# Kernel optimization log

Measured on AMD Instinct MI355X. Metric: run time of the kernel, lower is better.

## Reference

```python
import jax, jax.numpy as jnp
import numpy as np

N, C, H, W = 16, 64, 128, 128
SHIFT = 1  # frozen value of torch module's random.randint(-2, 2) drawn at __init__


def setup_inputs() -> dict:
    key = jax.random.key(0)
    k1, k2, k3 = jax.random.split(key, 3)
    x = jax.random.normal(k1, (N, C, H, W), dtype=jnp.float32)
    # p_3: Conv2d(c, c, (1,5), padding=(0,2), bias=False) -> weight (C_out, C_in, 1, 5)
    w3 = jax.random.normal(k2, (C, C, 1, 5), dtype=jnp.float32) * (1.0 / np.sqrt(5.0 * C))
    # p_7: Conv2d(9c, c, 1, groups=c, bias=False) -> per output channel, 9 input channels: (C, 9)
    w7 = jax.random.normal(k3, (C, 9), dtype=jnp.float32) * (1.0 / 3.0)
    return {"x": x, "w3": w3, "w7": w7}


def reference(x, w3, w7):
    n, c, h, w = x.shape
    # t_1: F.unfold(x, (1,3), dilation=(1,2), padding=(0,2)) -> width offsets -2, 0, +2 (zero padded)
    xp = jnp.pad(x, ((0, 0), (0, 0), (0, 0), (2, 2)))
    t1 = jnp.stack([xp[..., 0:w], xp[..., 2:w + 2], xp[..., 4:w + 4]], axis=2)  # (n,c,3,h,w)
    # t_3: 1x5 conv, padding (0,2)
    t3 = jax.lax.conv_general_dilated(
        x, w3, window_strides=(1, 1), padding=[(0, 0), (2, 2)],
        dimension_numbers=("NCHW", "OIHW", "NCHW"))  # (n,c,h,w)
    # t_4: F.unfold(t1 as (n,3c,h,w), (3,1), padding=(1,0)) -> height offsets -1, 0, +1
    t1p = jnp.pad(t1, ((0, 0), (0, 0), (0, 0), (1, 1), (0, 0)))
    t4 = jnp.stack([t1p[..., 0:h, :], t1p[..., 1:h + 1, :], t1p[..., 2:h + 2, :]],
                   axis=3)  # (n, c, 3[w_off], 3[h_off], h, w)
    # t_5: roll along the W axis (dim 5)
    t5 = jnp.roll(t4, SHIFT, axis=5)
    # t_6: maximum of lhs (n,c,1,3,h,w) and rhs (n,c,3,3,h,w); lhs offset dim aligns with rhs dim 3
    t6 = jnp.maximum(t1[:, :, None, :, :, :], t5)  # (n,c,3,3,h,w)
    # t_7: grouped 1x1 conv, groups=c, 9 input channels per group -> 1 output channel
    t6f = t6.reshape(n, c, 9, h, w)
    t7 = jnp.einsum("nckhw,ck->nchw", t6f, w7)
    return t7 * t3
```

## Files before the change

kernel.cpp:

```cpp
#include <hip/hip_runtime.h>

#define NN 16
#define CC 64
#define HH 128
#define WW 128

#define LDS_STRIDE 72
#define T3B_STRIDE 132

typedef __attribute__((ext_vector_type(8))) short short8;
typedef __attribute__((ext_vector_type(4))) float floatx4;

__device__ __forceinline__ short f2bf(float f) {
    union { float f; unsigned u; } v; v.f = f;
    unsigned r = v.u + 0x7fffu + ((v.u >> 16) & 1u);
    return (short)(r >> 16);
}
__device__ __forceinline__ unsigned pack2bf(float lo, float hi) {
    union { float f; unsigned u; } a, b; a.f = lo; b.f = hi;
    unsigned ra = a.u + 0x7fffu + ((a.u >> 16) & 1u);
    unsigned rb = b.u + 0x7fffu + ((b.u >> 16) & 1u);
    return (ra >> 16) | (rb & 0xffff0000u);
}
__device__ __forceinline__ float bf2f(unsigned short u) {
    union { unsigned u; float f; } v; v.u = ((unsigned)u) << 16;
    return v.f;
}

__global__ __launch_bounds__(256) void prep_w(const float* __restrict__ w3,
                                              short* __restrict__ Apk,
                                              float* __restrict__ zp) {
    int idx = blockIdx.x * 256 + threadIdx.x;
    if (idx < CC * 320) {
        int co = idx / 320;
        int kk = idx % 320;
        int mh = co >> 5, m = (co >> 4) & 1, lm = co & 15;
        int ks = kk >> 5, g = (kk >> 3) & 3, e = kk & 7;
        int tap = kk >> 6, ci = kk & 63;
        Apk[((((mh * 10 + ks) * 2 + m) * 64) + (g * 16 + lm)) * 8 + e] =
            f2bf(w3[(co * CC + ci) * 5 + tap]);
    }
    if (blockIdx.x == 0 && threadIdx.x < 64) zp[threadIdx.x] = 0.f;
}

__global__ __launch_bounds__(256, 6) void fused(const short* __restrict__ Apk,
                                                const float* __restrict__ x,
                                                const float* __restrict__ w7,
                                                const float* __restrict__ zp,
                                                float* __restrict__ out) {
    __shared__ __align__(16) char smem[19456];
    unsigned*    xsW  = (unsigned*)smem;
    const short* panel = (const short*)smem;
    short*       t3b  = (short*)smem;

    const int bid = blockIdx.x;
    const int nh  = ((bid & 7) << 8) | (bid >> 3);
    const int n   = nh >> 7;
    const int h   = nh & (HH - 1);
    const int tid = threadIdx.x;
    const int lane = tid & 63;
    const int W    = tid >> 6;

    {
        const int half = lane >> 5;
        const int wq   = lane & 31;
        const float* rowbase = x + ((size_t)n * CC * HH + h) * WW;
        #pragma unroll
        for (int i = 0; i < 4; ++i) {
            const int cp = W * 8 + i * 2 + half;
            const float* b0 = rowbase + (size_t)(2 * cp) * (HH * WW);
            float4 av = *(const float4*)(b0 + wq * 4);
            float4 bv = *(const float4*)(b0 + HH * WW + wq * 4);
            #pragma unroll
            for (int k = 0; k < 4; ++k) {
                int wp = wq * 4 + 2 + k;
                xsW[wp * 36 + cp] = pack2bf(av[k], bv[k]);
            }
        }
        if (tid < 128) {
            int wpi = tid >> 5;
            int wpz = (wpi < 2) ? wpi : 128 + wpi;
            xsW[wpz * 36 + (tid & 31)] = 0u;
        }
    }
    __syncthreads();

    const int lm = lane & 15;
    const int g  = lane >> 4;
    const int mh = W >> 1;
    const int wh = W & 1;

    floatx4 acc[2][4];
    #pragma unroll
    for (int m = 0; m < 2; ++m)
        #pragma unroll
        for (int j = 0; j < 4; ++j) acc[m][j] = (floatx4){0.f, 0.f, 0.f, 0.f};

    for (int ks = 0; ks < 10; ++ks) {
        const int kbase = ks * 32 + g * 8;
        const int tap   = kbase >> 6;
        const int cib   = kbase & 63;

        const short* ab = Apk + (((mh * 10 + ks) * 2) * 64 + lane) * 8;
        short8 a0 = *(const short8*)ab;
        short8 a1 = *(const short8*)(ab + 64 * 8);
        #pragma unroll
        for (int j = 0; j < 4; ++j) {
            int wp = (wh * 4 + j) * 16 + lm + tap;
            short8 b = *(const short8*)&panel[wp * LDS_STRIDE + cib];
            acc[0][j] = __builtin_amdgcn_mfma_f32_16x16x32_bf16(a0, b, acc[0][j], 0, 0, 0);
            acc[1][j] = __builtin_amdgcn_mfma_f32_16x16x32_bf16(a1, b, acc[1][j], 0, 0, 0);
        }
    }
    __syncthreads();

    #pragma unroll
    for (int m = 0; m < 2; ++m)
        #pragma unroll
        for (int j = 0; j < 4; ++j)
            #pragma unroll
            for (int r = 0; r < 4; ++r) {
                int co = (mh * 2 + m) * 16 + g * 4 + r;
                int w  = (wh * 4 + j) * 16 + lm;
                t3b[co * T3B_STRIDE + w] = f2bf(acc[m][j][r]);
            }

    const int w0   = (tid & 31) * 4;
    const int chi  = tid >> 5;
    const int lq31 = lane & 31;
    const bool isw = (lq31 == 0);
    const bool ise = (lq31 == 31);
    const int src31 = lane | 31;
    const int lsrc  = isw ? lane : lane - 1;
    const int rsrc  = ise ? lane : lane + 1;

    const float* pr[3]; int sr[3];
    const float* xb0 = x + (((size_t)(n * CC + chi)) * HH) * WW;
    #pragma unroll
    for (int r = 0; r < 3; ++r) {
        int hh = h + r - 1;
        bool hok = (unsigned)hh < HH;
        pr[r] = hok ? (xb0 + (size_t)hh * WW + w0) : zp;
        sr[r] = hok ? (8 * HH * WW) : 0;
    }
    const float* wcp = w7 + chi * 9;
    int t3o = chi * T3B_STRIDE + w0;
    float* outp = out + ((((size_t)(n * CC + chi)) * HH + h) * WW) + w0;

    __syncthreads();

    #define BUILD_WIN(dst, c)                                              \
        {                                                                  \
            float l1_ = __shfl((c).y, lsrc);                               \
            float l2_ = __shfl((c).z, lsrc);                               \
            float l3_ = __shfl((c).w, lsrc);                               \
            float r8_ = __shfl((c).x, rsrc);                               \
            float r9_ = __shfl((c).y, rsrc);                               \
            dst[1] = isw ? 0.f : l1_;                                      \
            dst[2] = isw ? 0.f : l2_;                                      \
            dst[3] = isw ? 0.f : l3_;                                      \
            dst[4] = (c).x; dst[5] = (c).y; dst[6] = (c).z; dst[7] = (c).w;\
            dst[8] = ise ? 0.f : r8_;                                      \
            dst[9] = ise ? 0.f : r9_;                                      \
        }

    #pragma unroll
    for (int it = 0; it < 8; ++it) {
        float4 cur[3];
        #pragma unroll
        for (int r = 0; r < 3; ++r) { cur[r] = *(const float4*)pr[r]; pr[r] += sr[r]; }
        float wc[9];
        #pragma unroll
        for (int t = 0; t < 9; ++t) wc[t] = wcp[t];
        ushort4 tv = *(const ushort4*)&t3b[t3o];

        float wrap0[3], wrap1[3];
        #pragma unroll
        for (int r = 0; r < 3; ++r) {
            wrap0[r] = __shfl(cur[r].y, src31);
            wrap1[r] = __shfl(cur[r].w, src31);
        }

        float win1[12];
        BUILD_WIN(win1, cur[1]);

        float t3v[4] = {bf2f(tv.x), bf2f(tv.y), bf2f(tv.z), bf2f(tv.w)};

        float res[4] = {0.f, 0.f, 0.f, 0.f};
        #pragma unroll
        for (int i = 0; i < 3; ++i) {
            float wini[12];
            if (i == 1) {
                #pragma unroll
                for (int t = 1; t < 10; ++t) wini[t] = win1[t];
            } else {
                BUILD_WIN(wini, cur[i]);
            }
            #pragma unroll
            for (int j = 0; j < 3; ++j) {
                #pragma unroll
                for (int e = 0; e < 4; ++e) {
                    float lhs = win1[e + 2 * i + 2];
                    float rhs = wini[e + 2 * j + 1];
                    if (e == 0)
                        rhs = isw ? ((j == 0) ? wrap0[i]
                                   : (j == 1) ? wrap1[i] : 0.f)
                                  : rhs;
                    res[e] = fmaf(wc[j * 3 + i], fmaxf(lhs, rhs), res[e]);
                }
            }
        }
        float4 o;
        o.x = res[0] * t3v[0]; o.y = res[1] * t3v[1];
        o.z = res[2] * t3v[2]; o.w = res[3] * t3v[3];
        *(float4*)outp = o;

        wcp  += 8 * 9;
        t3o  += 8 * T3B_STRIDE;
        outp += (size_t)8 * HH * WW;
    }
    #undef BUILD_WIN
}

extern "C" void kernel_launch(void* const* d_in, const int* in_sizes, int n_in,
                              void* d_out, int out_size, void* d_ws, size_t ws_size,
                              hipStream_t stream) {
    const float* x  = (const float*)d_in[0];
    const float* w3 = (const float*)d_in[1];
    const float* w7 = (const float*)d_in[2];
    float* out = (float*)d_out;

    short* Apk = (short*)d_ws;
    float* zp  = (float*)((char*)d_ws + 40960);

    prep_w<<<(CC * 320 + 255) / 256, 256, 0, stream>>>(w3, Apk, zp);
    fused<<<NN * HH, 256, 0, stream>>>(Apk, x, w7, zp, out);
}
```

Before: 140.3 us.

## Software-pipeline epilogue x loads, stage w7 in LDS, vectorize panel stores

The epilogue now issues the three x-row loads for the next channel group before computing the current one, using inline-asm global loads with explicit vmcnt waits. The first loads are issued before the barrier. The per-channel w7 weights are staged into LDS once per block and read back as vector loads instead of scalar global loads. The prologue loads 8 channels per thread and writes packed uint4 LDS stores instead of scalar ones. The manual waitcnt of 1 relies on the store-counter ordering, and the extra registers for double-buffering may lower occupancy.

Result: no change. 138.5 us (-1.3%).

```diff
diff --git a/kernel.cpp b/kernel.cpp
--- a/kernel.cpp
+++ b/kernel.cpp
@@ -7,6 +7,7 @@
 
 #define LDS_STRIDE 72
 #define T3B_STRIDE 132
+#define WCS_OFF    16896
 
 typedef __attribute__((ext_vector_type(8))) short short8;
 typedef __attribute__((ext_vector_type(4))) float floatx4;
@@ -25,6 +26,10 @@
 __device__ __forceinline__ float bf2f(unsigned short u) {
     union { unsigned u; float f; } v; v.u = ((unsigned)u) << 16;
     return v.f;
+}
+__device__ __forceinline__ void gload4(float4& d, const float* p) {
+    asm volatile("global_load_dwordx4 %0, %1, off"
+                 : "=&v"(d) : "v"(p) : "memory");
 }
 
 __global__ __launch_bounds__(256) void prep_w(const float* __restrict__ w3,
@@ -48,10 +53,11 @@
                                                 const float* __restrict__ w7,
                                                 const float* __restrict__ zp,
                                                 float* __restrict__ out) {
-    __shared__ __align__(16) char smem[19456];
+    __shared__ __align__(16) char smem[19968];
     unsigned*    xsW  = (unsigned*)smem;
     const short* panel = (const short*)smem;
     short*       t3b  = (short*)smem;
+    float*       wcs  = (float*)(smem + WCS_OFF);
 
     const int bid = blockIdx.x;
     const int nh  = ((bid & 7) << 8) | (bid >> 3);
@@ -64,18 +70,21 @@
     {
         const int half = lane >> 5;
         const int wq   = lane & 31;
-        const float* rowbase = x + ((size_t)n * CC * HH + h) * WW;
-        #pragma unroll
-        for (int i = 0; i < 4; ++i) {
-            const int cp = W * 8 + i * 2 + half;
-            const float* b0 = rowbase + (size_t)(2 * cp) * (HH * WW);
-            float4 av = *(const float4*)(b0 + wq * 4);
-            float4 bv = *(const float4*)(b0 + HH * WW + wq * 4);
-            #pragma unroll
-            for (int k = 0; k < 4; ++k) {
-                int wp = wq * 4 + 2 + k;
-                xsW[wp * 36 + cp] = pack2bf(av[k], bv[k]);
-            }
+        const int cp0  = W * 8 + half * 4;
+        const float* b0 = x + ((size_t)(n * CC + 2 * cp0) * HH + h) * WW;
+        float4 v[8];
+        #pragma unroll
+        for (int cc = 0; cc < 8; ++cc)
+            v[cc] = *(const float4*)(b0 + (size_t)cc * (HH * WW) + wq * 4);
+        #pragma unroll
+        for (int k = 0; k < 4; ++k) {
+            int wp = wq * 4 + 2 + k;
+            uint4 q;
+            q.x = pack2bf(v[0][k], v[1][k]);
+            q.y = pack2bf(v[2][k], v[3][k]);
+            q.z = pack2bf(v[4][k], v[5][k]);
+            q.w = pack2bf(v[6][k], v[7][k]);
+            *(uint4*)(xsW + wp * 36 + cp0) = q;
         }
         if (tid < 128) {
             int wpi = tid >> 5;
@@ -124,6 +133,15 @@
                 int w  = (wh * 4 + j) * 16 + lm;
                 t3b[co * T3B_STRIDE + w] = f2bf(acc[m][j][r]);
             }
+
+    if (tid < 144) {
+        float4 wv = *(const float4*)(w7 + tid * 4);
+        #pragma unroll
+        for (int e = 0; e < 4; ++e) {
+            int idx = tid * 4 + e;
+            wcs[(idx / 9) * 12 + (idx % 9)] = wv[e];
+        }
+    }
 
     const int w0   = (tid & 31) * 4;
     const int chi  = tid >> 5;
@@ -143,11 +161,17 @@
         pr[r] = hok ? (xb0 + (size_t)hh * WW + w0) : zp;
         sr[r] = hok ? (8 * HH * WW) : 0;
     }
-    const float* wcp = w7 + chi * 9;
     int t3o = chi * T3B_STRIDE + w0;
     float* outp = out + ((((size_t)(n * CC + chi)) * HH + h) * WW) + w0;
 
+    float4 curA, curB, curC;
+    gload4(curA, pr[0]); pr[0] += sr[0];
+    gload4(curB, pr[1]); pr[1] += sr[1];
+    gload4(curC, pr[2]); pr[2] += sr[2];
+
     __syncthreads();
+    asm volatile("s_waitcnt vmcnt(0)" ::: "memory");
+    __builtin_amdgcn_sched_barrier(0);
 
     #define BUILD_WIN(dst, c)                                              \
         {                                                                  \
@@ -166,13 +190,25 @@
 
     #pragma unroll
     for (int it = 0; it < 8; ++it) {
-        float4 cur[3];
-        #pragma unroll
-        for (int r = 0; r < 3; ++r) { cur[r] = *(const float4*)pr[r]; pr[r] += sr[r]; }
+        float4 nxtA, nxtB, nxtC;
+        if (it < 7) {
+            gload4(nxtA, pr[0]); pr[0] += sr[0];
+            gload4(nxtB, pr[1]); pr[1] += sr[1];
+            gload4(nxtC, pr[2]); pr[2] += sr[2];
+        }
+
+        const float* wrow = wcs + (it * 8 + chi) * 12;
         float wc[9];
-        #pragma unroll
-        for (int t = 0; t < 9; ++t) wc[t] = wcp[t];
+        {
+            float4 wv0 = *(const float4*)wrow;
+            float4 wv1 = *(const float4*)(wrow + 4);
+            wc[0] = wv0.x; wc[1] = wv0.y; wc[2] = wv0.z; wc[3] = wv0.w;
+            wc[4] = wv1.x; wc[5] = wv1.y; wc[6] = wv1.z; wc[7] = wv1.w;
+            wc[8] = wrow[8];
+        }
         ushort4 tv = *(const ushort4*)&t3b[t3o];
+
+        float4 cur[3] = {curA, curB, curC};
 
         float wrap0[3], wrap1[3];
         #pragma unroll
@@ -215,9 +251,14 @@
         o.z = res[2] * t3v[2]; o.w = res[3] * t3v[3];
         *(float4*)outp = o;
 
-        wcp  += 8 * 9;
         t3o  += 8 * T3B_STRIDE;
         outp += (size_t)8 * HH * WW;
+
+        if (it < 7) {
+            asm volatile("s_waitcnt vmcnt(1)" ::: "memory");
+            __builtin_amdgcn_sched_barrier(0);
+            curA = nxtA; curB = nxtB; curC = nxtC;
+        }
     }
     #undef BUILD_WIN
 }
```
